# Kernel optimization log

Hardware: AMD Instinct MI355X
Metric: run time of the kernel (lower is better)

The kernel has to match this reference:

```python
import jax, jax.numpy as jnp
import numpy as np
from jax import lax

THETA = 0.7
DN = ('NCHW', 'OIHW', 'NCHW')


def setup_inputs() -> dict:
    key = jax.random.key(0)
    k1, k2 = jax.random.split(key)
    x = jax.random.normal(k1, (16, 64, 128, 128), dtype=jnp.float32)
    W = jax.random.normal(k2, (64, 64, 3, 3), dtype=jnp.float32) * 0.05
    return {"x": x, "W": W}


def _shift_sum(x):
    # Sum of the center view plus the 8 shifted views of the reflection-padded
    # input (the original code's lt/mt/rt/lm/center/mr/ld/md/rd slices cover
    # exactly the full 3x3 neighborhood of the padded tensor).
    B, C, H, W_ = x.shape
    xp = jnp.pad(x, ((0, 0), (0, 0), (1, 1), (1, 1)), mode='reflect')
    s = jnp.zeros_like(x)
    for dy in range(3):
        for dx in range(3):
            s = s + xp[:, :, dy:dy + H, dx:dx + W_]
    return s


def reference(x, W):
    # Conv is linear and bias=False, so sum_i conv(shift_i(x)) == conv(sum_i shift_i(x)).
    s = _shift_sum(x)  # [B,C,H,W]
    out_normal = lax.conv_general_dilated(s, W, (1, 1), [(1, 1), (1, 1)], dimension_numbers=DN)
    kernel_diff = W.sum(axis=(2, 3))[:, :, None, None]  # [C_out,C_in,1,1]
    out_diff = lax.conv_general_dilated(s, kernel_diff, (1, 1), [(0, 0), (0, 0)], dimension_numbers=DN)
    return out_normal - THETA * out_diff
```

## Files before the change

### kernel.cpp

```cpp
#include <hip/hip_runtime.h>
#include <stdint.h>


#define THETA 0.7f

typedef __attribute__((ext_vector_type(8))) short bf16x8;
typedef __attribute__((ext_vector_type(16))) float f32x16;

__device__ inline unsigned short f2bf(float f) {
    unsigned u = __float_as_uint(f);
    u = (u + 0x7FFFu + ((u >> 16) & 1u)) >> 16;
    return (unsigned short)u;
}

__global__ void weff_kernel(const float* __restrict__ W, unsigned short* __restrict__ Wt2) {
    int t = blockIdx.x * blockDim.x + threadIdx.x;
    if (t >= 512) return;
    int o = t >> 3;
    int ch8 = t & 7;
    int c0 = ch8 * 8;
    int ic = ch8 >> 1;
    int mf = o >> 5;
    int lane = (o & 31) | ((ch8 & 1) << 5);

    float v[8][9];
    float tsum[8];
#pragma unroll
    for (int j = 0; j < 8; j++) {
        const float* w = W + ((size_t)o * 64 + c0 + j) * 9;
        float sum = 0.f;
#pragma unroll
        for (int k = 0; k < 9; k++) { v[j][k] = w[k]; sum += v[j][k]; }
        tsum[j] = sum;
    }
#pragma unroll
    for (int tap = 0; tap < 9; tap++) {
        unsigned short* dst = Wt2 + (((size_t)(tap * 4 + ic) * 2 + mf) * 64 + lane) * 8;
#pragma unroll
        for (int j = 0; j < 8; j++) {
            float val = v[j][tap] - ((tap == 4) ? THETA * tsum[j] : 0.f);
            dst[j] = f2bf(val);
        }
    }
}

__global__ __launch_bounds__(512, 2) void fused_kernel(const float* __restrict__ x,
                                                       const unsigned short* __restrict__ Wt2,
                                                       float* __restrict__ out) {
    __shared__ __align__(16) unsigned short sS[6 * 132 * 64];

    int bid = blockIdx.x;
    int b = bid >> 5;
    int h0 = (bid & 31) * 4;
    int tid = threadIdx.x;
    int lane = tid & 63;
    int wv = tid >> 6;
    int n32 = lane & 31;
    int q2 = lane >> 5;
    int orow = wv >> 1;
    int whalf = wv & 1;

    int4 z = make_int4(0, 0, 0, 0);
    if (tid < 96) {
        int rr = tid >> 4;
        int sl = ((tid & 15) >> 3) ? 129 : 0;
        int g = tid & 7;
        *(int4*)((char*)sS + ((size_t)(rr * 132 + sl) * 8 + g) * 16) = z;
    }
    if (h0 == 0)
        for (int i = tid; i < 1056; i += 512) *(int4*)((char*)sS + (size_t)i * 16) = z;
    if (h0 == 124)
        for (int i = tid; i < 1056; i += 512) *(int4*)((char*)sS + (size_t)(5280 + i) * 16) = z;

    bf16x8 Af[8], An[8];
#pragma unroll
    for (int ic = 0; ic < 4; ic++)
#pragma unroll
        for (int mf = 0; mf < 2; mf++)
            Af[ic * 2 + mf] = *(const bf16x8*)(Wt2 + (((size_t)(0 * 4 + ic) * 2 + mf) * 64 + lane) * 8);

    {
        int w4 = tid & 31;
        int cg = tid >> 5;
        int c0 = cg * 4;
        int u8 = cg >> 1;
        int hh = (cg & 1) * 4;
        const float* xp = x + ((size_t)(b * 64 + c0)) * 16384 + w4 * 4;

        int hgf = (h0 == 0) ? 0 : h0 - 1;
        int hm = (hgf == 0) ? 1 : hgf - 1;
        float4 A[4], Bv[4], C[4];
#pragma unroll
        for (int cc = 0; cc < 4; cc++) {
            A[cc]  = *(const float4*)(xp + (size_t)cc * 16384 + (size_t)hm * 128);
            Bv[cc] = *(const float4*)(xp + (size_t)cc * 16384 + (size_t)hgf * 128);
            C[cc]  = *(const float4*)(xp + (size_t)cc * 16384 + (size_t)(hgf + 1) * 128);
        }

#pragma unroll
        for (int rr = 0; rr < 6; rr++) {
            int hg = h0 - 1 + rr;
            if (hg < 0 || hg > 127) continue;

            float4 Cn[4];
            if (rr < 5) {
                int hn = hg + 2;
                if (hn > 127) hn = 126;
#pragma unroll
                for (int cc = 0; cc < 4; cc++)
                    Cn[cc] = *(const float4*)(xp + (size_t)cc * 16384 + (size_t)hn * 128);
            }

            unsigned short res[4][4];
#pragma unroll
            for (int cc = 0; cc < 4; cc++) {
                float4 vs;
                vs.x = A[cc].x + Bv[cc].x + C[cc].x;
                vs.y = A[cc].y + Bv[cc].y + C[cc].y;
                vs.z = A[cc].z + Bv[cc].z + C[cc].z;
                vs.w = A[cc].w + Bv[cc].w + C[cc].w;
                float L = __shfl_up(vs.w, 1, 32);
                float R = __shfl_down(vs.x, 1, 32);
                float sx = (w4 == 0) ? vs.x + 2.f * vs.y : L + vs.x + vs.y;
                float sy = vs.x + vs.y + vs.z;
                float sz = vs.y + vs.z + vs.w;
                float sw_ = (w4 == 31) ? 2.f * vs.z + vs.w : vs.z + vs.w + R;
                res[cc][0] = f2bf(sx);
                res[cc][1] = f2bf(sy);
                res[cc][2] = f2bf(sz);
                res[cc][3] = f2bf(sw_);
            }
#pragma unroll
            for (int k = 0; k < 4; k++) {
                int slot = w4 * 4 + k + 1;
                ushort4 o4 = make_ushort4(res[0][k], res[1][k], res[2][k], res[3][k]);
                *(ushort4*)(sS + (size_t)(rr * 132 + slot) * 64 + ((u8 ^ (slot & 7)) << 3) + hh) = o4;
            }
            if (rr < 5) {
#pragma unroll
                for (int cc = 0; cc < 4; cc++) { A[cc] = Bv[cc]; Bv[cc] = C[cc]; C[cc] = Cn[cc]; }
            }
        }
    }
    __syncthreads();

    int p0[3][4];
#pragma unroll
    for (int kx = 0; kx < 3; kx++)
#pragma unroll
        for (int ic = 0; ic < 4; ic++) {
            int slot = n32 + kx + whalf * 64;
            int g = (ic * 2 + q2) ^ (slot & 7);
            p0[kx][ic] = slot * 64 + g * 8;
        }

    f32x16 acc[2][2];
#pragma unroll
    for (int mf = 0; mf < 2; mf++)
#pragma unroll
        for (int nf = 0; nf < 2; nf++)
#pragma unroll
            for (int r = 0; r < 16; r++) acc[mf][nf][r] = 0.f;

#pragma unroll
    for (int tap = 0; tap < 9; tap++) {
        int ky = tap / 3, kx = tap % 3;
        if (tap < 8) {
#pragma unroll
            for (int ic = 0; ic < 4; ic++)
#pragma unroll
                for (int mf = 0; mf < 2; mf++)
                    An[ic * 2 + mf] = *(const bf16x8*)(Wt2 + (((size_t)((tap + 1) * 4 + ic) * 2 + mf) * 64 + lane) * 8);
        }
#pragma unroll
        for (int ic = 0; ic < 4; ic++) {
            const unsigned short* bp = sS + (size_t)(orow + ky) * 8448 + p0[kx][ic];
            bf16x8 b0 = *(const bf16x8*)(bp);
            bf16x8 b1 = *(const bf16x8*)(bp + 2048);
            acc[0][0] = __builtin_amdgcn_mfma_f32_32x32x16_bf16(Af[ic * 2 + 0], b0, acc[0][0], 0, 0, 0);
            acc[0][1] = __builtin_amdgcn_mfma_f32_32x32x16_bf16(Af[ic * 2 + 0], b1, acc[0][1], 0, 0, 0);
            acc[1][0] = __builtin_amdgcn_mfma_f32_32x32x16_bf16(Af[ic * 2 + 1], b0, acc[1][0], 0, 0, 0);
            acc[1][1] = __builtin_amdgcn_mfma_f32_32x32x16_bf16(Af[ic * 2 + 1], b1, acc[1][1], 0, 0, 0);
        }
        if (tap < 8) {
#pragma unroll
            for (int k = 0; k < 8; k++) Af[k] = An[k];
        }
    }

    float* ob = out + ((size_t)b * 64) * 16384 + (size_t)(h0 + orow) * 128 + whalf * 64;
#pragma unroll
    for (int mf = 0; mf < 2; mf++)
#pragma unroll
        for (int nf = 0; nf < 2; nf++)
#pragma unroll
            for (int r = 0; r < 16; r++) {
                int o = mf * 32 + (r & 3) + 8 * (r >> 2) + 4 * q2;
                ob[(size_t)o * 16384 + nf * 32 + n32] = acc[mf][nf][r];
            }
}

extern "C" void kernel_launch(void* const* d_in, const int* in_sizes, int n_in,
                              void* d_out, int out_size, void* d_ws, size_t ws_size,
                              hipStream_t stream) {
    const float* x = (const float*)d_in[0];
    const float* W = (const float*)d_in[1];
    float* outp = (float*)d_out;

    unsigned short* Wt2 = (unsigned short*)d_ws;

    weff_kernel<<<2, 256, 0, stream>>>(W, Wt2);
    fused_kernel<<<512, 512, 0, stream>>>(x, Wt2, outp);
}
```

Baseline: 142.9 us.

## Halve rows per block and split output channels across waves for occupancy

Each block now produces 2 output rows instead of 4, so the shared tile shrinks from 6 to 4 halo rows and the grid doubles to 1024 blocks. The 8 waves are split over output-channel halves, rows and width halves, so each wave holds one weight fragment set and two accumulators instead of four. Launch bounds go to 4 blocks per CU to raise occupancy and cut register pressure. The cost is more halo recomputation (2 extra input rows per 2 output rows instead of per 4), redundant shared-tile building, and fewer MFMAs per B-fragment load.

```diff
diff --git a/kernel.cpp b/kernel.cpp
--- a/kernel.cpp
+++ b/kernel.cpp
@@ -44,40 +44,39 @@
     }
 }
 
-__global__ __launch_bounds__(512, 2) void fused_kernel(const float* __restrict__ x,
+__global__ __launch_bounds__(512, 4) void fused_kernel(const float* __restrict__ x,
                                                        const unsigned short* __restrict__ Wt2,
                                                        float* __restrict__ out) {
-    __shared__ __align__(16) unsigned short sS[6 * 132 * 64];
+    __shared__ __align__(16) unsigned short sS[4 * 132 * 64];
 
     int bid = blockIdx.x;
-    int b = bid >> 5;
-    int h0 = (bid & 31) * 4;
+    int b = bid >> 6;
+    int h0 = (bid & 63) * 2;
     int tid = threadIdx.x;
     int lane = tid & 63;
     int wv = tid >> 6;
     int n32 = lane & 31;
     int q2 = lane >> 5;
-    int orow = wv >> 1;
+    int ohalf = wv >> 2;
+    int orow = (wv >> 1) & 1;
     int whalf = wv & 1;
 
     int4 z = make_int4(0, 0, 0, 0);
-    if (tid < 96) {
+    if (tid < 64) {
         int rr = tid >> 4;
-        int sl = ((tid & 15) >> 3) ? 129 : 0;
+        int sl = ((tid >> 3) & 1) ? 129 : 0;
         int g = tid & 7;
         *(int4*)((char*)sS + ((size_t)(rr * 132 + sl) * 8 + g) * 16) = z;
     }
     if (h0 == 0)
         for (int i = tid; i < 1056; i += 512) *(int4*)((char*)sS + (size_t)i * 16) = z;
-    if (h0 == 124)
-        for (int i = tid; i < 1056; i += 512) *(int4*)((char*)sS + (size_t)(5280 + i) * 16) = z;
-
-    bf16x8 Af[8], An[8];
+    if (h0 == 126)
+        for (int i = tid; i < 1056; i += 512) *(int4*)((char*)sS + (size_t)(3168 + i) * 16) = z;
+
+    bf16x8 Af[4], An[4];
 #pragma unroll
     for (int ic = 0; ic < 4; ic++)
-#pragma unroll
-        for (int mf = 0; mf < 2; mf++)
-            Af[ic * 2 + mf] = *(const bf16x8*)(Wt2 + (((size_t)(0 * 4 + ic) * 2 + mf) * 64 + lane) * 8);
+        Af[ic] = *(const bf16x8*)(Wt2 + (((size_t)(0 * 4 + ic) * 2 + ohalf) * 64 + lane) * 8);
 
     {
         int w4 = tid & 31;
@@ -98,12 +97,12 @@
         }
 
 #pragma unroll
-        for (int rr = 0; rr < 6; rr++) {
+        for (int rr = 0; rr < 4; rr++) {
             int hg = h0 - 1 + rr;
             if (hg < 0 || hg > 127) continue;
 
             float4 Cn[4];
-            if (rr < 5) {
+            if (rr < 3) {
                 int hn = hg + 2;
                 if (hn > 127) hn = 126;
 #pragma unroll
@@ -136,7 +135,7 @@
                 ushort4 o4 = make_ushort4(res[0][k], res[1][k], res[2][k], res[3][k]);
                 *(ushort4*)(sS + (size_t)(rr * 132 + slot) * 64 + ((u8 ^ (slot & 7)) << 3) + hh) = o4;
             }
-            if (rr < 5) {
+            if (rr < 3) {
 #pragma unroll
                 for (int cc = 0; cc < 4; cc++) { A[cc] = Bv[cc]; Bv[cc] = C[cc]; C[cc] = Cn[cc]; }
             }
@@ -154,13 +153,11 @@
             p0[kx][ic] = slot * 64 + g * 8;
         }
 
-    f32x16 acc[2][2];
-#pragma unroll
-    for (int mf = 0; mf < 2; mf++)
-#pragma unroll
-        for (int nf = 0; nf < 2; nf++)
-#pragma unroll
-            for (int r = 0; r < 16; r++) acc[mf][nf][r] = 0.f;
+    f32x16 acc[2];
+#pragma unroll
+    for (int nf = 0; nf < 2; nf++)
+#pragma unroll
+        for (int r = 0; r < 16; r++) acc[nf][r] = 0.f;
 
 #pragma unroll
     for (int tap = 0; tap < 9; tap++) {
@@ -168,36 +165,30 @@
         if (tap < 8) {
 #pragma unroll
             for (int ic = 0; ic < 4; ic++)
-#pragma unroll
-                for (int mf = 0; mf < 2; mf++)
-                    An[ic * 2 + mf] = *(const bf16x8*)(Wt2 + (((size_t)((tap + 1) * 4 + ic) * 2 + mf) * 64 + lane) * 8);
+                An[ic] = *(const bf16x8*)(Wt2 + (((size_t)((tap + 1) * 4 + ic) * 2 + ohalf) * 64 + lane) * 8);
         }
 #pragma unroll
         for (int ic = 0; ic < 4; ic++) {
             const unsigned short* bp = sS + (size_t)(orow + ky) * 8448 + p0[kx][ic];
             bf16x8 b0 = *(const bf16x8*)(bp);
             bf16x8 b1 = *(const bf16x8*)(bp + 2048);
-            acc[0][0] = __builtin_amdgcn_mfma_f32_32x32x16_bf16(Af[ic * 2 + 0], b0, acc[0][0], 0, 0, 0);
-            acc[0][1] = __builtin_amdgcn_mfma_f32_32x32x16_bf16(Af[ic * 2 + 0], b1, acc[0][1], 0, 0, 0);
-            acc[1][0] = __builtin_amdgcn_mfma_f32_32x32x16_bf16(Af[ic * 2 + 1], b0, acc[1][0], 0, 0, 0);
-            acc[1][1] = __builtin_amdgcn_mfma_f32_32x32x16_bf16(Af[ic * 2 + 1], b1, acc[1][1], 0, 0, 0);
+            acc[0] = __builtin_amdgcn_mfma_f32_32x32x16_bf16(Af[ic], b0, acc[0], 0, 0, 0);
+            acc[1] = __builtin_amdgcn_mfma_f32_32x32x16_bf16(Af[ic], b1, acc[1], 0, 0, 0);
         }
         if (tap < 8) {
 #pragma unroll
-            for (int k = 0; k < 8; k++) Af[k] = An[k];
+            for (int k = 0; k < 4; k++) Af[k] = An[k];
         }
     }
 
     float* ob = out + ((size_t)b * 64) * 16384 + (size_t)(h0 + orow) * 128 + whalf * 64;
 #pragma unroll
-    for (int mf = 0; mf < 2; mf++)
-#pragma unroll
-        for (int nf = 0; nf < 2; nf++)
-#pragma unroll
-            for (int r = 0; r < 16; r++) {
-                int o = mf * 32 + (r & 3) + 8 * (r >> 2) + 4 * q2;
-                ob[(size_t)o * 16384 + nf * 32 + n32] = acc[mf][nf][r];
-            }
+    for (int nf = 0; nf < 2; nf++)
+#pragma unroll
+        for (int r = 0; r < 16; r++) {
+            int o = ohalf * 32 + (r & 3) + 8 * (r >> 2) + 4 * q2;
+            ob[(size_t)o * 16384 + nf * 32 + n32] = acc[nf][r];
+        }
 }
 
 extern "C" void kernel_launch(void* const* d_in, const int* in_sizes, int n_in,
@@ -210,5 +201,5 @@
     unsigned short* Wt2 = (unsigned short*)d_ws;
 
     weff_kernel<<<2, 256, 0, stream>>>(W, Wt2);
-    fused_kernel<<<512, 512, 0, stream>>>(x, Wt2, outp);
-}
+    fused_kernel<<<1024, 512, 0, stream>>>(x, Wt2, outp);
+}
```

New measurement: 141.2 us. About the same (-1.2%).
